# Kernel tuning notes

Measured on AMD Instinct MI355X. Metric: run time of the kernel, lower is better.

## Reference

```python
import jax, jax.numpy as jnp
import numpy as np

HIDDEN = 256
NUM_CLASSES = 96
ENC_FEAT = 256


def setup_inputs() -> dict:
    key = jax.random.key(0)
    ks = jax.random.split(key, 12)
    B, T, D, H, C = 1024, 64, ENC_FEAT, HIDDEN, NUM_CLASSES
    s = 0.05
    return {
        "batch_H": jax.random.normal(ks[0], (B, T, D), jnp.float32),
        "text": jax.random.randint(ks[1], (B, 26), 0, C, jnp.int64),
        "batch_max_length": 25,
        # attention cell params
        "Wi2h": jax.random.normal(ks[2], (D, H), jnp.float32) * s,
        "Wh2h": jax.random.normal(ks[3], (H, H), jnp.float32) * s,
        "bh2h": jnp.zeros((H,), jnp.float32),
        "w_score": jax.random.normal(ks[4], (H, 1), jnp.float32) * s,
        # LSTMCell params (keras gate order: i, f, c, o)
        "Wx": jax.random.normal(ks[5], (D + C, 4 * H), jnp.float32) * s,
        "Wh": jax.random.normal(ks[6], (H, 4 * H), jnp.float32) * s,
        "b_lstm": jnp.concatenate([jnp.zeros((H,)), jnp.ones((H,)), jnp.zeros((2 * H,))]).astype(jnp.float32),
        # generator
        "Wg": jax.random.normal(ks[7], (H, C), jnp.float32) * s,
        "bg": jnp.zeros((C,), jnp.float32),
    }


def _decode(batch_H, text, num_steps, Wi2h, Wh2h, bh2h, w_score, Wx, Wh, b_lstm, Wg, bg):
    B = batch_H.shape[0]
    H = Wh.shape[0]
    C = Wg.shape[1]
    # precompute encoder projection once: [B, T, H]
    batch_H_proj = jnp.einsum("btd,dh->bth", batch_H, Wi2h)

    def step(carry, char_idx):
        h, c = carry
        onehot = jax.nn.one_hot(char_idx, C, dtype=batch_H.dtype)  # [B, C]
        # Bahdanau score: tanh(Wi2h*H + Wh2h*h) @ w_score -> [B, T, 1]
        hp = (h @ Wh2h + bh2h)[:, None, :]
        e = jnp.tanh(batch_H_proj + hp) @ w_score
        alpha = jax.nn.softmax(e, axis=1)  # [B, T, 1]
        context = jnp.sum(alpha * batch_H, axis=1)  # [B, D]
        x = jnp.concatenate([context, onehot], axis=1)  # [B, D+C]
        gates = x @ Wx + h @ Wh + b_lstm  # [B, 4H]
        i_g, f_g, g_g, o_g = jnp.split(gates, 4, axis=1)
        c_new = jax.nn.sigmoid(f_g) * c + jax.nn.sigmoid(i_g) * jnp.tanh(g_g)
        h_new = jax.nn.sigmoid(o_g) * jnp.tanh(c_new)
        return (h_new, c_new), h_new

    h0 = jnp.zeros((B, H), batch_H.dtype)
    c0 = jnp.zeros((B, H), batch_H.dtype)
    chars = text[:, :num_steps].T  # [num_steps, B]
    _, hiddens = jax.lax.scan(step, (h0, c0), chars)
    output_hiddens = jnp.transpose(hiddens, (1, 0, 2))  # [B, num_steps, H]
    probs = output_hiddens @ Wg + bg  # [B, num_steps, C]
    return probs


def reference(batch_H, text, batch_max_length, Wi2h, Wh2h, bh2h, w_score, Wx, Wh, b_lstm, Wg, bg):
    num_steps = batch_max_length + 1
    return _decode(batch_H, text, num_steps, Wi2h, Wh2h, bh2h, w_score, Wx, Wh, b_lstm, Wg, bg)
```

## Files before the change

### kernel.cpp

```cpp
#include <hip/hip_runtime.h>
#include <hip/hip_bf16.h>

constexpr int B  = 1024;
constexpr int T  = 64;
constexpr int D  = 256;
constexpr int H  = 256;
constexpr int C  = 96;
constexpr int NS = 26;
constexpr int G  = 4 * H;

__device__ __forceinline__ float fsig(float x) {
    return __builtin_amdgcn_rcpf(1.0f + __expf(-x));
}
__device__ __forceinline__ float ftanh(float x) {
    float e = __expf(2.0f * x);
    return fmaf(-2.0f, __builtin_amdgcn_rcpf(e + 1.0f), 1.0f);
}
__device__ __forceinline__ float bf_lo(unsigned int p) {
    union { unsigned int i; float f; } v;
    v.i = p << 16;
    return v.f;
}
__device__ __forceinline__ float bf_hi(unsigned int p) {
    union { unsigned int i; float f; } v;
    v.i = p & 0xFFFF0000u;
    return v.f;
}
__device__ __forceinline__ unsigned short f2bf(float f) {
    __hip_bfloat16 h = __float2bfloat16(f);
    return *reinterpret_cast<unsigned short*>(&h);
}

__global__ __launch_bounds__(256) void cvt_kernel(
        const float* __restrict__ in, ushort* __restrict__ out) {
    const int i = blockIdx.x * 256 + threadIdx.x;
    const float4 v = reinterpret_cast<const float4*>(in)[i];
    ushort4 o;
    o.x = f2bf(v.x); o.y = f2bf(v.y); o.z = f2bf(v.z); o.w = f2bf(v.w);
    reinterpret_cast<ushort4*>(out)[i] = o;
}

__global__ __launch_bounds__(256) void proj_kernel(
        const float* __restrict__ bH, const float* __restrict__ Wi2h,
        ushort* __restrict__ proj) {
    __shared__ float xs[32 * 256];
    const int row0 = blockIdx.x * 32;
    const int tid = threadIdx.x;

    const float4* src = reinterpret_cast<const float4*>(bH + (size_t)row0 * D);
    float4* dst = reinterpret_cast<float4*>(xs);
#pragma unroll
    for (int i = 0; i < 8; ++i) dst[tid + 256 * i] = src[tid + 256 * i];
    __syncthreads();

    const int wv = tid >> 6, lane = tid & 63;
    const int r0 = wv * 8;
    const int c0 = lane * 4;
    float4 acc[8];
#pragma unroll
    for (int r = 0; r < 8; ++r) acc[r] = make_float4(0.f, 0.f, 0.f, 0.f);

    for (int k = 0; k < D; k += 4) {
        const float4 w0 = *reinterpret_cast<const float4*>(&Wi2h[(k + 0) * H + c0]);
        const float4 w1 = *reinterpret_cast<const float4*>(&Wi2h[(k + 1) * H + c0]);
        const float4 w2 = *reinterpret_cast<const float4*>(&Wi2h[(k + 2) * H + c0]);
        const float4 w3 = *reinterpret_cast<const float4*>(&Wi2h[(k + 3) * H + c0]);
#pragma unroll
        for (int r = 0; r < 8; ++r) {
            const float4 x = *reinterpret_cast<const float4*>(&xs[(r0 + r) * 256 + k]);
            acc[r].x = fmaf(x.x, w0.x, fmaf(x.y, w1.x, fmaf(x.z, w2.x, fmaf(x.w, w3.x, acc[r].x))));
            acc[r].y = fmaf(x.x, w0.y, fmaf(x.y, w1.y, fmaf(x.z, w2.y, fmaf(x.w, w3.y, acc[r].y))));
            acc[r].z = fmaf(x.x, w0.z, fmaf(x.y, w1.z, fmaf(x.z, w2.z, fmaf(x.w, w3.z, acc[r].z))));
            acc[r].w = fmaf(x.x, w0.w, fmaf(x.y, w1.w, fmaf(x.z, w2.w, fmaf(x.w, w3.w, acc[r].w))));
        }
    }
#pragma unroll
    for (int r = 0; r < 8; ++r) {
        const int brow = row0 + r0 + r;
        const int bb = brow >> 6, tt = brow & 63;
        ushort4 o;
        o.x = f2bf(acc[r].x); o.y = f2bf(acc[r].y);
        o.z = f2bf(acc[r].z); o.w = f2bf(acc[r].w);
        *reinterpret_cast<ushort4*>(
            &proj[(size_t)bb * H * T + (c0 >> 3) * (T * 8) + tt * 8 + (c0 & 7)]) = o;
    }
}

__global__ __launch_bounds__(512, 2) void decoder_kernel(
        const ushort* __restrict__ proj, const ushort* __restrict__ bHb,
        const int* __restrict__ text, const float* __restrict__ Wx,
        const float* __restrict__ Wh, const float* __restrict__ b_lstm,
        const float* __restrict__ Wh2h, const float* __restrict__ bh2h,
        const float* __restrict__ w_score, float* __restrict__ hiddens) {
    __shared__ float hp_s[4][256];
    __shared__ float h_s[4][256];
    __shared__ float c_s[4][256];
    __shared__ float ctx_s[4][256];
    __shared__ float gates[4][1024];
    __shared__ float alpha_s[4][64];
    __shared__ float ws_s[256];

    const int row0 = blockIdx.x * 4;
    const int tid = threadIdx.x;
    const int wv = tid >> 6, lane = tid & 63;

    for (int i = tid; i < 1024; i += 512) {
        const int r = i >> 8, j = i & 255;
        h_s[r][j] = 0.0f;
        c_s[r][j] = 0.0f;
        hp_s[r][j] = bh2h[j];
    }
    if (tid < 256) ws_s[tid] = w_score[tid];
    __syncthreads();

    for (int t = 0; t < NS; ++t) {
        if (wv < 4) {
            const int r = wv;
            const ushort* pb = proj + (size_t)(row0 + r) * H * T + lane * 8;
            float e = 0.0f;
#pragma unroll 4
            for (int h = 0; h < H; h += 8) {
                const uint4 pv = *reinterpret_cast<const uint4*>(pb + (h >> 3) * (T * 8));
                const float4 hp0 = *reinterpret_cast<const float4*>(&hp_s[r][h]);
                const float4 hp1 = *reinterpret_cast<const float4*>(&hp_s[r][h + 4]);
                const float4 w0 = *reinterpret_cast<const float4*>(&ws_s[h]);
                const float4 w1 = *reinterpret_cast<const float4*>(&ws_s[h + 4]);
                e += ftanh(bf_lo(pv.x) + hp0.x) * w0.x;
                e += ftanh(bf_hi(pv.x) + hp0.y) * w0.y;
                e += ftanh(bf_lo(pv.y) + hp0.z) * w0.z;
                e += ftanh(bf_hi(pv.y) + hp0.w) * w0.w;
                e += ftanh(bf_lo(pv.z) + hp1.x) * w1.x;
                e += ftanh(bf_hi(pv.z) + hp1.y) * w1.y;
                e += ftanh(bf_lo(pv.w) + hp1.z) * w1.z;
                e += ftanh(bf_hi(pv.w) + hp1.w) * w1.w;
            }
            {
                float m = e;
#pragma unroll
                for (int off = 32; off > 0; off >>= 1) m = fmaxf(m, __shfl_xor(m, off));
                const float p = __expf(e - m);
                float sum = p;
#pragma unroll
                for (int off = 32; off > 0; off >>= 1) sum += __shfl_xor(sum, off);
                alpha_s[r][lane] = p * __builtin_amdgcn_rcpf(sum);
            }
            {
                const ushort* xb = bHb + (size_t)(row0 + r) * T * D + lane * 4;
                float4 cacc = make_float4(0.f, 0.f, 0.f, 0.f);
#pragma unroll 8
                for (int tt = 0; tt < T; ++tt) {
                    const ushort4 x4 = *reinterpret_cast<const ushort4*>(xb + tt * D);
                    const float av = alpha_s[r][tt];
                    cacc.x = fmaf(av, bf_lo((unsigned)x4.x), cacc.x);
                    cacc.y = fmaf(av, bf_lo((unsigned)x4.y), cacc.y);
                    cacc.z = fmaf(av, bf_lo((unsigned)x4.z), cacc.z);
                    cacc.w = fmaf(av, bf_lo((unsigned)x4.w), cacc.w);
                }
                *reinterpret_cast<float4*>(&ctx_s[r][lane * 4]) = cacc;
            }
        } else {
            const int cw = (wv - 4) * 256 + lane * 4;
            float4 a0, a1, a2, a3;
            {
                const float4 bb = *reinterpret_cast<const float4*>(&b_lstm[cw]);
                const int ch0 = text[(row0 + 0) * NS + t];
                const int ch1 = text[(row0 + 1) * NS + t];
                const int ch2 = text[(row0 + 2) * NS + t];
                const int ch3 = text[(row0 + 3) * NS + t];
                const float4 o0 = *reinterpret_cast<const float4*>(&Wx[(size_t)(D + ch0) * G + cw]);
                const float4 o1 = *reinterpret_cast<const float4*>(&Wx[(size_t)(D + ch1) * G + cw]);
                const float4 o2 = *reinterpret_cast<const float4*>(&Wx[(size_t)(D + ch2) * G + cw]);
                const float4 o3 = *reinterpret_cast<const float4*>(&Wx[(size_t)(D + ch3) * G + cw]);
                a0 = make_float4(bb.x + o0.x, bb.y + o0.y, bb.z + o0.z, bb.w + o0.w);
                a1 = make_float4(bb.x + o1.x, bb.y + o1.y, bb.z + o1.z, bb.w + o1.w);
                a2 = make_float4(bb.x + o2.x, bb.y + o2.y, bb.z + o2.z, bb.w + o2.w);
                a3 = make_float4(bb.x + o3.x, bb.y + o3.y, bb.z + o3.z, bb.w + o3.w);
            }
            for (int k = 0; k < H; k += 4) {
                const float4 w0 = *reinterpret_cast<const float4*>(&Wh[(size_t)(k + 0) * G + cw]);
                const float4 w1 = *reinterpret_cast<const float4*>(&Wh[(size_t)(k + 1) * G + cw]);
                const float4 w2 = *reinterpret_cast<const float4*>(&Wh[(size_t)(k + 2) * G + cw]);
                const float4 w3 = *reinterpret_cast<const float4*>(&Wh[(size_t)(k + 3) * G + cw]);
                const float4 x0 = *reinterpret_cast<const float4*>(&h_s[0][k]);
                const float4 x1 = *reinterpret_cast<const float4*>(&h_s[1][k]);
                const float4 x2 = *reinterpret_cast<const float4*>(&h_s[2][k]);
                const float4 x3 = *reinterpret_cast<const float4*>(&h_s[3][k]);
#define ACC4(A, X)                                                              \
    A.x = fmaf(X.x, w0.x, fmaf(X.y, w1.x, fmaf(X.z, w2.x, fmaf(X.w, w3.x, A.x)))); \
    A.y = fmaf(X.x, w0.y, fmaf(X.y, w1.y, fmaf(X.z, w2.y, fmaf(X.w, w3.y, A.y)))); \
    A.z = fmaf(X.x, w0.z, fmaf(X.y, w1.z, fmaf(X.z, w2.z, fmaf(X.w, w3.z, A.z)))); \
    A.w = fmaf(X.x, w0.w, fmaf(X.y, w1.w, fmaf(X.z, w2.w, fmaf(X.w, w3.w, A.w))))
                ACC4(a0, x0);
                ACC4(a1, x1);
                ACC4(a2, x2);
                ACC4(a3, x3);
#undef ACC4
            }
            *reinterpret_cast<float4*>(&gates[0][cw]) = a0;
            *reinterpret_cast<float4*>(&gates[1][cw]) = a1;
            *reinterpret_cast<float4*>(&gates[2][cw]) = a2;
            *reinterpret_cast<float4*>(&gates[3][cw]) = a3;
        }
        __syncthreads();

        {
            const int cw = wv * 128 + lane * 2;
            float2 a0 = *reinterpret_cast<float2*>(&gates[0][cw]);
            float2 a1 = *reinterpret_cast<float2*>(&gates[1][cw]);
            float2 a2 = *reinterpret_cast<float2*>(&gates[2][cw]);
            float2 a3 = *reinterpret_cast<float2*>(&gates[3][cw]);
            for (int k = 0; k < D; k += 4) {
                const float2 w0 = *reinterpret_cast<const float2*>(&Wx[(size_t)(k + 0) * G + cw]);
                const float2 w1 = *reinterpret_cast<const float2*>(&Wx[(size_t)(k + 1) * G + cw]);
                const float2 w2 = *reinterpret_cast<const float2*>(&Wx[(size_t)(k + 2) * G + cw]);
                const float2 w3 = *reinterpret_cast<const float2*>(&Wx[(size_t)(k + 3) * G + cw]);
                const float4 x0 = *reinterpret_cast<const float4*>(&ctx_s[0][k]);
                const float4 x1 = *reinterpret_cast<const float4*>(&ctx_s[1][k]);
                const float4 x2 = *reinterpret_cast<const float4*>(&ctx_s[2][k]);
                const float4 x3 = *reinterpret_cast<const float4*>(&ctx_s[3][k]);
#define ACC2(A, X)                                                              \
    A.x = fmaf(X.x, w0.x, fmaf(X.y, w1.x, fmaf(X.z, w2.x, fmaf(X.w, w3.x, A.x)))); \
    A.y = fmaf(X.x, w0.y, fmaf(X.y, w1.y, fmaf(X.z, w2.y, fmaf(X.w, w3.y, A.y))))
                ACC2(a0, x0);
                ACC2(a1, x1);
                ACC2(a2, x2);
                ACC2(a3, x3);
#undef ACC2
            }
            *reinterpret_cast<float2*>(&gates[0][cw]) = a0;
            *reinterpret_cast<float2*>(&gates[1][cw]) = a1;
            *reinterpret_cast<float2*>(&gates[2][cw]) = a2;
            *reinterpret_cast<float2*>(&gates[3][cw]) = a3;
        }
        __syncthreads();

#pragma unroll
        for (int pp = 0; pp < 2; ++pp) {
            const int r = (tid >> 8) + pp * 2;
            const int j = tid & 255;
            const float gi = gates[r][j];
            const float gf = gates[r][256 + j];
            const float gc = gates[r][512 + j];
            const float go = gates[r][768 + j];
            const float cv = fsig(gf) * c_s[r][j] + fsig(gi) * ftanh(gc);
            c_s[r][j] = cv;
            const float hvv = fsig(go) * ftanh(cv);
            h_s[r][j] = hvv;
            hiddens[((size_t)(row0 + r) * NS + t) * H + j] = hvv;
        }
        __syncthreads();

        {
            const int j = tid & 255;
            const int rb = (tid >> 8) * 2;
            float acc0 = bh2h[j];
            float acc1 = acc0;
            for (int k = 0; k < H; k += 4) {
                const float w0 = Wh2h[(k + 0) * H + j];
                const float w1 = Wh2h[(k + 1) * H + j];
                const float w2 = Wh2h[(k + 2) * H + j];
                const float w3 = Wh2h[(k + 3) * H + j];
                const float4 xa = *reinterpret_cast<const float4*>(&h_s[rb][k]);
                const float4 xb = *reinterpret_cast<const float4*>(&h_s[rb + 1][k]);
                acc0 = fmaf(xa.x, w0, fmaf(xa.y, w1, fmaf(xa.z, w2, fmaf(xa.w, w3, acc0))));
                acc1 = fmaf(xb.x, w0, fmaf(xb.y, w1, fmaf(xb.z, w2, fmaf(xb.w, w3, acc1))));
            }
            hp_s[rb][j] = acc0;
            hp_s[rb + 1][j] = acc1;
        }
        __syncthreads();
    }
}

__global__ __launch_bounds__(192) void gen_kernel(
        const float* __restrict__ hiddens, const float* __restrict__ Wg,
        const float* __restrict__ bg, float* __restrict__ out) {
    const int row0 = blockIdx.x * 16 + (threadIdx.x / 96) * 8;
    const int cc = threadIdx.x % 96;
    float acc[8];
    const float bias = bg[cc];
#pragma unroll
    for (int r = 0; r < 8; ++r) acc[r] = bias;
    for (int k = 0; k < H; k += 4) {
        const float w0 = Wg[(k + 0) * C + cc];
        const float w1 = Wg[(k + 1) * C + cc];
        const float w2 = Wg[(k + 2) * C + cc];
        const float w3 = Wg[(k + 3) * C + cc];
#pragma unroll
        for (int r = 0; r < 8; ++r) {
            const float4 x = *reinterpret_cast<const float4*>(
                &hiddens[(size_t)(row0 + r) * H + k]);
            acc[r] = fmaf(x.x, w0, acc[r]);
            acc[r] = fmaf(x.y, w1, acc[r]);
            acc[r] = fmaf(x.z, w2, acc[r]);
            acc[r] = fmaf(x.w, w3, acc[r]);
        }
    }
#pragma unroll
    for (int r = 0; r < 8; ++r) out[(size_t)(row0 + r) * C + cc] = acc[r];
}

extern "C" void kernel_launch(void* const* d_in, const int* in_sizes, int n_in,
                              void* d_out, int out_size, void* d_ws, size_t ws_size,
                              hipStream_t stream) {
    const float* batch_H = (const float*)d_in[0];
    const int*   text    = (const int*)d_in[1];
    const float* Wi2h    = (const float*)d_in[3];
    const float* Wh2h    = (const float*)d_in[4];
    const float* bh2h    = (const float*)d_in[5];
    const float* w_score = (const float*)d_in[6];
    const float* Wx      = (const float*)d_in[7];
    const float* Wh      = (const float*)d_in[8];
    const float* b_lstm  = (const float*)d_in[9];
    const float* Wg      = (const float*)d_in[10];
    const float* bg      = (const float*)d_in[11];
    float* out = (float*)d_out;

    char* wsb = (char*)d_ws;
    ushort* proj_bf = (ushort*)wsb;
    ushort* bH_bf   = (ushort*)(wsb + (size_t)B * T * H * 2);
    float*  hiddens = (float*)(wsb + (size_t)B * T * H * 2 * 2);

    cvt_kernel<<<B * T * D / 4 / 256, 256, 0, stream>>>(batch_H, bH_bf);
    proj_kernel<<<B * T / 32, 256, 0, stream>>>(batch_H, Wi2h, proj_bf);
    decoder_kernel<<<B / 4, 512, 0, stream>>>(proj_bf, bH_bf, text, Wx, Wh, b_lstm,
                                              Wh2h, bh2h, w_score, hiddens);
    gen_kernel<<<B * NS / 16, 192, 0, stream>>>(hiddens, Wg, bg, out);
}
```

Baseline: 1.406 ms.

## Pack LSTM weights to bf16 k-pairs and split Wx GEMV across all warps

Adds a pre-pass that converts Wh and the context rows of Wx into bf16, interleaved in k-pairs, so each lane loads 4 columns × 2 k-values in one 16-byte load. Both LSTM gate matvecs in the decoder now read this packed bf16 weight with 8-deep load batching, halving weight bytes streamed per step. The Wx context product is split over k between two warp halves, with a new shared partial buffer summed in the cell update. Unroll factors also increase in the score and Wh2h loops. This risks bf16 rounding error in the recurrent weights and adds shared memory that may affect occupancy.

```diff
diff --git a/kernel.cpp b/kernel.cpp
--- a/kernel.cpp
+++ b/kernel.cpp
@@ -38,6 +38,16 @@
     ushort4 o;
     o.x = f2bf(v.x); o.y = f2bf(v.y); o.z = f2bf(v.z); o.w = f2bf(v.w);
     reinterpret_cast<ushort4*>(out)[i] = o;
+}
+
+__global__ __launch_bounds__(256) void pack_w_kernel(
+        const float* __restrict__ W, ushort* __restrict__ P) {
+    const int i = blockIdx.x * 256 + threadIdx.x;
+    const int k2 = i >> 10, col = i & 1023;
+    ushort2 o;
+    o.x = f2bf(W[(size_t)(2 * k2) * G + col]);
+    o.y = f2bf(W[(size_t)(2 * k2 + 1) * G + col]);
+    *reinterpret_cast<ushort2*>(&P[(size_t)i * 2]) = o;
 }
 
 __global__ __launch_bounds__(256) void proj_kernel(
@@ -89,14 +99,16 @@
 __global__ __launch_bounds__(512, 2) void decoder_kernel(
         const ushort* __restrict__ proj, const ushort* __restrict__ bHb,
         const int* __restrict__ text, const float* __restrict__ Wx,
-        const float* __restrict__ Wh, const float* __restrict__ b_lstm,
-        const float* __restrict__ Wh2h, const float* __restrict__ bh2h,
-        const float* __restrict__ w_score, float* __restrict__ hiddens) {
+        const ushort* __restrict__ WhP, const ushort* __restrict__ WxP,
+        const float* __restrict__ b_lstm, const float* __restrict__ Wh2h,
+        const float* __restrict__ bh2h, const float* __restrict__ w_score,
+        float* __restrict__ hiddens) {
     __shared__ float hp_s[4][256];
     __shared__ float h_s[4][256];
     __shared__ float c_s[4][256];
     __shared__ float ctx_s[4][256];
     __shared__ float gates[4][1024];
+    __shared__ float gpart[4][1024];
     __shared__ float alpha_s[4][64];
     __shared__ float ws_s[256];
 
@@ -118,7 +130,7 @@
             const int r = wv;
             const ushort* pb = proj + (size_t)(row0 + r) * H * T + lane * 8;
             float e = 0.0f;
-#pragma unroll 4
+#pragma unroll 8
             for (int h = 0; h < H; h += 8) {
                 const uint4 pv = *reinterpret_cast<const uint4*>(pb + (h >> 3) * (T * 8));
                 const float4 hp0 = *reinterpret_cast<const float4*>(&hp_s[r][h]);
@@ -176,25 +188,31 @@
                 a2 = make_float4(bb.x + o2.x, bb.y + o2.y, bb.z + o2.z, bb.w + o2.w);
                 a3 = make_float4(bb.x + o3.x, bb.y + o3.y, bb.z + o3.z, bb.w + o3.w);
             }
-            for (int k = 0; k < H; k += 4) {
-                const float4 w0 = *reinterpret_cast<const float4*>(&Wh[(size_t)(k + 0) * G + cw]);
-                const float4 w1 = *reinterpret_cast<const float4*>(&Wh[(size_t)(k + 1) * G + cw]);
-                const float4 w2 = *reinterpret_cast<const float4*>(&Wh[(size_t)(k + 2) * G + cw]);
-                const float4 w3 = *reinterpret_cast<const float4*>(&Wh[(size_t)(k + 3) * G + cw]);
-                const float4 x0 = *reinterpret_cast<const float4*>(&h_s[0][k]);
-                const float4 x1 = *reinterpret_cast<const float4*>(&h_s[1][k]);
-                const float4 x2 = *reinterpret_cast<const float4*>(&h_s[2][k]);
-                const float4 x3 = *reinterpret_cast<const float4*>(&h_s[3][k]);
-#define ACC4(A, X)                                                              \
-    A.x = fmaf(X.x, w0.x, fmaf(X.y, w1.x, fmaf(X.z, w2.x, fmaf(X.w, w3.x, A.x)))); \
-    A.y = fmaf(X.x, w0.y, fmaf(X.y, w1.y, fmaf(X.z, w2.y, fmaf(X.w, w3.y, A.y)))); \
-    A.z = fmaf(X.x, w0.z, fmaf(X.y, w1.z, fmaf(X.z, w2.z, fmaf(X.w, w3.z, A.z)))); \
-    A.w = fmaf(X.x, w0.w, fmaf(X.y, w1.w, fmaf(X.z, w2.w, fmaf(X.w, w3.w, A.w))))
-                ACC4(a0, x0);
-                ACC4(a1, x1);
-                ACC4(a2, x2);
-                ACC4(a3, x3);
-#undef ACC4
+            const ushort* wp = WhP + (size_t)cw * 2;
+            for (int kc = 0; kc < 128; kc += 8) {
+                uint4 pv[8];
+#pragma unroll
+                for (int u = 0; u < 8; ++u)
+                    pv[u] = *reinterpret_cast<const uint4*>(wp + (size_t)(kc + u) * 2048);
+#pragma unroll
+                for (int u = 0; u < 8; ++u) {
+                    const int k0 = (kc + u) * 2;
+                    const float2 x0 = *reinterpret_cast<const float2*>(&h_s[0][k0]);
+                    const float2 x1 = *reinterpret_cast<const float2*>(&h_s[1][k0]);
+                    const float2 x2 = *reinterpret_cast<const float2*>(&h_s[2][k0]);
+                    const float2 x3 = *reinterpret_cast<const float2*>(&h_s[3][k0]);
+                    const float wl0 = bf_lo(pv[u].x), whh0 = bf_hi(pv[u].x);
+                    const float wl1 = bf_lo(pv[u].y), whh1 = bf_hi(pv[u].y);
+                    const float wl2 = bf_lo(pv[u].z), whh2 = bf_hi(pv[u].z);
+                    const float wl3 = bf_lo(pv[u].w), whh3 = bf_hi(pv[u].w);
+#define GACC(A, X)                                      \
+    A.x = fmaf(X.x, wl0, fmaf(X.y, whh0, A.x));         \
+    A.y = fmaf(X.x, wl1, fmaf(X.y, whh1, A.y));         \
+    A.z = fmaf(X.x, wl2, fmaf(X.y, whh2, A.z));         \
+    A.w = fmaf(X.x, wl3, fmaf(X.y, whh3, A.w));
+                    GACC(a0, x0) GACC(a1, x1) GACC(a2, x2) GACC(a3, x3)
+#undef GACC
+                }
             }
             *reinterpret_cast<float4*>(&gates[0][cw]) = a0;
             *reinterpret_cast<float4*>(&gates[1][cw]) = a1;
@@ -204,33 +222,49 @@
         __syncthreads();
 
         {
-            const int cw = wv * 128 + lane * 2;
-            float2 a0 = *reinterpret_cast<float2*>(&gates[0][cw]);
-            float2 a1 = *reinterpret_cast<float2*>(&gates[1][cw]);
-            float2 a2 = *reinterpret_cast<float2*>(&gates[2][cw]);
-            float2 a3 = *reinterpret_cast<float2*>(&gates[3][cw]);
-            for (int k = 0; k < D; k += 4) {
-                const float2 w0 = *reinterpret_cast<const float2*>(&Wx[(size_t)(k + 0) * G + cw]);
-                const float2 w1 = *reinterpret_cast<const float2*>(&Wx[(size_t)(k + 1) * G + cw]);
-                const float2 w2 = *reinterpret_cast<const float2*>(&Wx[(size_t)(k + 2) * G + cw]);
-                const float2 w3 = *reinterpret_cast<const float2*>(&Wx[(size_t)(k + 3) * G + cw]);
-                const float4 x0 = *reinterpret_cast<const float4*>(&ctx_s[0][k]);
-                const float4 x1 = *reinterpret_cast<const float4*>(&ctx_s[1][k]);
-                const float4 x2 = *reinterpret_cast<const float4*>(&ctx_s[2][k]);
-                const float4 x3 = *reinterpret_cast<const float4*>(&ctx_s[3][k]);
-#define ACC2(A, X)                                                              \
-    A.x = fmaf(X.x, w0.x, fmaf(X.y, w1.x, fmaf(X.z, w2.x, fmaf(X.w, w3.x, A.x)))); \
-    A.y = fmaf(X.x, w0.y, fmaf(X.y, w1.y, fmaf(X.z, w2.y, fmaf(X.w, w3.y, A.y))))
-                ACC2(a0, x0);
-                ACC2(a1, x1);
-                ACC2(a2, x2);
-                ACC2(a3, x3);
-#undef ACC2
-            }
-            *reinterpret_cast<float2*>(&gates[0][cw]) = a0;
-            *reinterpret_cast<float2*>(&gates[1][cw]) = a1;
-            *reinterpret_cast<float2*>(&gates[2][cw]) = a2;
-            *reinterpret_cast<float2*>(&gates[3][cw]) = a3;
+            const int cw2 = (wv & 3) * 256 + lane * 4;
+            const int kb = (wv < 4) ? 0 : 64;
+            float4 b0 = make_float4(0.f, 0.f, 0.f, 0.f), b1 = b0, b2 = b0, b3 = b0;
+            const ushort* wp = WxP + (size_t)cw2 * 2 + (size_t)kb * 2048;
+            for (int kc = 0; kc < 64; kc += 8) {
+                uint4 pv[8];
+#pragma unroll
+                for (int u = 0; u < 8; ++u)
+                    pv[u] = *reinterpret_cast<const uint4*>(wp + (size_t)(kc + u) * 2048);
+#pragma unroll
+                for (int u = 0; u < 8; ++u) {
+                    const int k0 = (kb + kc + u) * 2;
+                    const float2 x0 = *reinterpret_cast<const float2*>(&ctx_s[0][k0]);
+                    const float2 x1 = *reinterpret_cast<const float2*>(&ctx_s[1][k0]);
+                    const float2 x2 = *reinterpret_cast<const float2*>(&ctx_s[2][k0]);
+                    const float2 x3 = *reinterpret_cast<const float2*>(&ctx_s[3][k0]);
+                    const float wl0 = bf_lo(pv[u].x), whh0 = bf_hi(pv[u].x);
+                    const float wl1 = bf_lo(pv[u].y), whh1 = bf_hi(pv[u].y);
+                    const float wl2 = bf_lo(pv[u].z), whh2 = bf_hi(pv[u].z);
+                    const float wl3 = bf_lo(pv[u].w), whh3 = bf_hi(pv[u].w);
+#define GACC(A, X)                                      \
+    A.x = fmaf(X.x, wl0, fmaf(X.y, whh0, A.x));         \
+    A.y = fmaf(X.x, wl1, fmaf(X.y, whh1, A.y));         \
+    A.z = fmaf(X.x, wl2, fmaf(X.y, whh2, A.z));         \
+    A.w = fmaf(X.x, wl3, fmaf(X.y, whh3, A.w));
+                    GACC(b0, x0) GACC(b1, x1) GACC(b2, x2) GACC(b3, x3)
+#undef GACC
+                }
+            }
+            if (wv < 4) {
+#pragma unroll
+                for (int r = 0; r < 4; ++r) {
+                    const float4 br = (r == 0) ? b0 : (r == 1) ? b1 : (r == 2) ? b2 : b3;
+                    float4 g = *reinterpret_cast<float4*>(&gates[r][cw2]);
+                    g.x += br.x; g.y += br.y; g.z += br.z; g.w += br.w;
+                    *reinterpret_cast<float4*>(&gates[r][cw2]) = g;
+                }
+            } else {
+                *reinterpret_cast<float4*>(&gpart[0][cw2]) = b0;
+                *reinterpret_cast<float4*>(&gpart[1][cw2]) = b1;
+                *reinterpret_cast<float4*>(&gpart[2][cw2]) = b2;
+                *reinterpret_cast<float4*>(&gpart[3][cw2]) = b3;
+            }
         }
         __syncthreads();
 
@@ -238,10 +272,10 @@
         for (int pp = 0; pp < 2; ++pp) {
             const int r = (tid >> 8) + pp * 2;
             const int j = tid & 255;
-            const float gi = gates[r][j];
-            const float gf = gates[r][256 + j];
-            const float gc = gates[r][512 + j];
-            const float go = gates[r][768 + j];
+            const float gi = gates[r][j] + gpart[r][j];
+            const float gf = gates[r][256 + j] + gpart[r][256 + j];
+            const float gc = gates[r][512 + j] + gpart[r][512 + j];
+            const float go = gates[r][768 + j] + gpart[r][768 + j];
             const float cv = fsig(gf) * c_s[r][j] + fsig(gi) * ftanh(gc);
             c_s[r][j] = cv;
             const float hvv = fsig(go) * ftanh(cv);
@@ -255,6 +289,7 @@
             const int rb = (tid >> 8) * 2;
             float acc0 = bh2h[j];
             float acc1 = acc0;
+#pragma unroll 4
             for (int k = 0; k < H; k += 4) {
                 const float w0 = Wh2h[(k + 0) * H + j];
                 const float w1 = Wh2h[(k + 1) * H + j];
@@ -320,10 +355,15 @@
     ushort* proj_bf = (ushort*)wsb;
     ushort* bH_bf   = (ushort*)(wsb + (size_t)B * T * H * 2);
     float*  hiddens = (float*)(wsb + (size_t)B * T * H * 2 * 2);
+    ushort* WhP     = (ushort*)(wsb + (size_t)B * T * H * 2 * 2 +
+                                (size_t)B * NS * H * 4);
+    ushort* WxP     = WhP + (size_t)(H / 2) * G * 2;
 
     cvt_kernel<<<B * T * D / 4 / 256, 256, 0, stream>>>(batch_H, bH_bf);
+    pack_w_kernel<<<(H / 2) * G / 256, 256, 0, stream>>>(Wh, WhP);
+    pack_w_kernel<<<(D / 2) * G / 256, 256, 0, stream>>>(Wx, WxP);
     proj_kernel<<<B * T / 32, 256, 0, stream>>>(batch_H, Wi2h, proj_bf);
-    decoder_kernel<<<B / 4, 512, 0, stream>>>(proj_bf, bH_bf, text, Wx, Wh, b_lstm,
-                                              Wh2h, bh2h, w_score, hiddens);
+    decoder_kernel<<<B / 4, 512, 0, stream>>>(proj_bf, bH_bf, text, Wx, WhP, WxP,
+                                              b_lstm, Wh2h, bh2h, w_score, hiddens);
     gen_kernel<<<B * NS / 16, 192, 0, stream>>>(hiddens, Wg, bg, out);
 }
```

Measured after the change: 1.278 ms. 9.1% less time.

## Use bf16 MFMA with hi/lo split for decoder recurrent matmuls

Applied to the files above, without the earlier changes.

Replaces the scalar FP32 FMA loops for the Wh, Wx-context and Wh2h matmuls inside the decoder step with 16x16x32 bf16 MFMA instructions. Weights are pre-packed into fragment layout by a new pack kernel, and activations are split into bf16 hi and lo parts stored in swizzled shared memory so that near-FP32 accuracy is kept. The bias and one-hot contributions move into the elementwise gate stage. This is meant to cut per-step ALU and weight-load cost. In exchange it doubles the MFMA work through the hi/lo split and pads the 4-row tiles up to 16 rows, so most of each MFMA is wasted.

```diff
diff --git a/kernel.cpp b/kernel.cpp
--- a/kernel.cpp
+++ b/kernel.cpp
@@ -9,6 +9,11 @@
 constexpr int NS = 26;
 constexpr int G  = 4 * H;
 
+typedef __attribute__((ext_vector_type(8))) short short8v;
+typedef __attribute__((ext_vector_type(4))) float f32x4;
+
+#define MFMA16 __builtin_amdgcn_mfma_f32_16x16x32_bf16
+
 __device__ __forceinline__ float fsig(float x) {
     return __builtin_amdgcn_rcpf(1.0f + __expf(-x));
 }
@@ -17,14 +22,10 @@
     return fmaf(-2.0f, __builtin_amdgcn_rcpf(e + 1.0f), 1.0f);
 }
 __device__ __forceinline__ float bf_lo(unsigned int p) {
-    union { unsigned int i; float f; } v;
-    v.i = p << 16;
-    return v.f;
+    union { unsigned int i; float f; } v; v.i = p << 16; return v.f;
 }
 __device__ __forceinline__ float bf_hi(unsigned int p) {
-    union { unsigned int i; float f; } v;
-    v.i = p & 0xFFFF0000u;
-    return v.f;
+    union { unsigned int i; float f; } v; v.i = p & 0xFFFF0000u; return v.f;
 }
 __device__ __forceinline__ unsigned short f2bf(float f) {
     __hip_bfloat16 h = __float2bfloat16(f);
@@ -38,6 +39,22 @@
     ushort4 o;
     o.x = f2bf(v.x); o.y = f2bf(v.y); o.z = f2bf(v.z); o.w = f2bf(v.w);
     reinterpret_cast<ushort4*>(out)[i] = o;
+}
+
+__global__ __launch_bounds__(256) void pack_frag_kernel(
+        const float* __restrict__ W, ushort* __restrict__ WF,
+        int ncol_tiles, int wstride) {
+    const int i = blockIdx.x * 256 + threadIdx.x;
+    const int l = i & 63;
+    const int s = (i >> 6) & 7;
+    const int ct = i >> 9;
+    if (ct >= ncol_tiles) return;
+    const int col = ct * 16 + (l & 15);
+    const int k0 = s * 32 + (l >> 4) * 8;
+    ushort o[8];
+#pragma unroll
+    for (int j = 0; j < 8; ++j) o[j] = f2bf(W[(size_t)(k0 + j) * wstride + col]);
+    *reinterpret_cast<uint4*>(&WF[(size_t)i * 8]) = *reinterpret_cast<uint4*>(o);
 }
 
 __global__ __launch_bounds__(256) void proj_kernel(
@@ -86,27 +103,54 @@
     }
 }
 
+__device__ __forceinline__ short8v ldA(const ushort* base, int lane, int s) {
+    const int row = lane & 15, g = lane >> 4;
+    const int byte = ((row << 9) + (s << 6) + (g << 4)) ^ ((row & 7) << 4);
+    return *reinterpret_cast<const short8v*>(
+        reinterpret_cast<const char*>(base) + byte);
+}
+__device__ __forceinline__ void loadB(short8v dst[8], const ushort* __restrict__ wf,
+                                      int ctg, int lane) {
+#pragma unroll
+    for (int s = 0; s < 8; ++s)
+        dst[s] = *reinterpret_cast<const short8v*>(
+            wf + (((size_t)ctg * 8 + s) * 64 + lane) * 8);
+}
+__device__ __forceinline__ f32x4 mfma_hilo(const short8v aHi[8], const short8v aLo[8],
+                                           const short8v b[8]) {
+    f32x4 acc = {0.f, 0.f, 0.f, 0.f};
+#pragma unroll
+    for (int s = 0; s < 8; ++s) {
+        acc = MFMA16(aLo[s], b[s], acc, 0, 0, 0);
+        acc = MFMA16(aHi[s], b[s], acc, 0, 0, 0);
+    }
+    return acc;
+}
+
 __global__ __launch_bounds__(512, 2) void decoder_kernel(
         const ushort* __restrict__ proj, const ushort* __restrict__ bHb,
         const int* __restrict__ text, const float* __restrict__ Wx,
-        const float* __restrict__ Wh, const float* __restrict__ b_lstm,
-        const float* __restrict__ Wh2h, const float* __restrict__ bh2h,
-        const float* __restrict__ w_score, float* __restrict__ hiddens) {
+        const ushort* __restrict__ WhF, const ushort* __restrict__ WxF,
+        const ushort* __restrict__ Wh2hF, const float* __restrict__ b_lstm,
+        const float* __restrict__ bh2h, const float* __restrict__ w_score,
+        float* __restrict__ hiddens) {
     __shared__ float hp_s[4][256];
-    __shared__ float h_s[4][256];
     __shared__ float c_s[4][256];
-    __shared__ float ctx_s[4][256];
     __shared__ float gates[4][1024];
     __shared__ float alpha_s[4][64];
     __shared__ float ws_s[256];
+    __shared__ ushort hHi[16 * 256], hLo[16 * 256];
+    __shared__ ushort cHi[16 * 256], cLo[16 * 256];
 
     const int row0 = blockIdx.x * 4;
     const int tid = threadIdx.x;
     const int wv = tid >> 6, lane = tid & 63;
 
+    for (int i = tid; i < 4096; i += 512) {
+        hHi[i] = 0; hLo[i] = 0; cHi[i] = 0; cLo[i] = 0;
+    }
     for (int i = tid; i < 1024; i += 512) {
         const int r = i >> 8, j = i & 255;
-        h_s[r][j] = 0.0f;
         c_s[r][j] = 0.0f;
         hp_s[r][j] = bh2h[j];
     }
@@ -118,7 +162,7 @@
             const int r = wv;
             const ushort* pb = proj + (size_t)(row0 + r) * H * T + lane * 8;
             float e = 0.0f;
-#pragma unroll 4
+#pragma unroll 8
             for (int h = 0; h < H; h += 8) {
                 const uint4 pv = *reinterpret_cast<const uint4*>(pb + (h >> 3) * (T * 8));
                 const float4 hp0 = *reinterpret_cast<const float4*>(&hp_s[r][h]);
@@ -156,81 +200,66 @@
                     cacc.z = fmaf(av, bf_lo((unsigned)x4.z), cacc.z);
                     cacc.w = fmaf(av, bf_lo((unsigned)x4.w), cacc.w);
                 }
-                *reinterpret_cast<float4*>(&ctx_s[r][lane * 4]) = cacc;
+                ushort4 hi, lo;
+                hi.x = f2bf(cacc.x); lo.x = f2bf(cacc.x - bf_lo((unsigned)hi.x));
+                hi.y = f2bf(cacc.y); lo.y = f2bf(cacc.y - bf_lo((unsigned)hi.y));
+                hi.z = f2bf(cacc.z); lo.z = f2bf(cacc.z - bf_lo((unsigned)hi.z));
+                hi.w = f2bf(cacc.w); lo.w = f2bf(cacc.w - bf_lo((unsigned)hi.w));
+                const int byte = ((r << 9) + (lane << 3)) ^ ((r & 7) << 4);
+                *reinterpret_cast<ushort4*>(reinterpret_cast<char*>(cHi) + byte) = hi;
+                *reinterpret_cast<ushort4*>(reinterpret_cast<char*>(cLo) + byte) = lo;
             }
         } else {
-            const int cw = (wv - 4) * 256 + lane * 4;
-            float4 a0, a1, a2, a3;
-            {
-                const float4 bb = *reinterpret_cast<const float4*>(&b_lstm[cw]);
-                const int ch0 = text[(row0 + 0) * NS + t];
-                const int ch1 = text[(row0 + 1) * NS + t];
-                const int ch2 = text[(row0 + 2) * NS + t];
-                const int ch3 = text[(row0 + 3) * NS + t];
-                const float4 o0 = *reinterpret_cast<const float4*>(&Wx[(size_t)(D + ch0) * G + cw]);
-                const float4 o1 = *reinterpret_cast<const float4*>(&Wx[(size_t)(D + ch1) * G + cw]);
-                const float4 o2 = *reinterpret_cast<const float4*>(&Wx[(size_t)(D + ch2) * G + cw]);
-                const float4 o3 = *reinterpret_cast<const float4*>(&Wx[(size_t)(D + ch3) * G + cw]);
-                a0 = make_float4(bb.x + o0.x, bb.y + o0.y, bb.z + o0.z, bb.w + o0.w);
-                a1 = make_float4(bb.x + o1.x, bb.y + o1.y, bb.z + o1.z, bb.w + o1.w);
-                a2 = make_float4(bb.x + o2.x, bb.y + o2.y, bb.z + o2.z, bb.w + o2.w);
-                a3 = make_float4(bb.x + o3.x, bb.y + o3.y, bb.z + o3.z, bb.w + o3.w);
-            }
-            for (int k = 0; k < H; k += 4) {
-                const float4 w0 = *reinterpret_cast<const float4*>(&Wh[(size_t)(k + 0) * G + cw]);
-                const float4 w1 = *reinterpret_cast<const float4*>(&Wh[(size_t)(k + 1) * G + cw]);
-                const float4 w2 = *reinterpret_cast<const float4*>(&Wh[(size_t)(k + 2) * G + cw]);
-                const float4 w3 = *reinterpret_cast<const float4*>(&Wh[(size_t)(k + 3) * G + cw]);
-                const float4 x0 = *reinterpret_cast<const float4*>(&h_s[0][k]);
-                const float4 x1 = *reinterpret_cast<const float4*>(&h_s[1][k]);
-                const float4 x2 = *reinterpret_cast<const float4*>(&h_s[2][k]);
-                const float4 x3 = *reinterpret_cast<const float4*>(&h_s[3][k]);
-#define ACC4(A, X)                                                              \
-    A.x = fmaf(X.x, w0.x, fmaf(X.y, w1.x, fmaf(X.z, w2.x, fmaf(X.w, w3.x, A.x)))); \
-    A.y = fmaf(X.x, w0.y, fmaf(X.y, w1.y, fmaf(X.z, w2.y, fmaf(X.w, w3.y, A.y)))); \
-    A.z = fmaf(X.x, w0.z, fmaf(X.y, w1.z, fmaf(X.z, w2.z, fmaf(X.w, w3.z, A.z)))); \
-    A.w = fmaf(X.x, w0.w, fmaf(X.y, w1.w, fmaf(X.z, w2.w, fmaf(X.w, w3.w, A.w))))
-                ACC4(a0, x0);
-                ACC4(a1, x1);
-                ACC4(a2, x2);
-                ACC4(a3, x3);
-#undef ACC4
-            }
-            *reinterpret_cast<float4*>(&gates[0][cw]) = a0;
-            *reinterpret_cast<float4*>(&gates[1][cw]) = a1;
-            *reinterpret_cast<float4*>(&gates[2][cw]) = a2;
-            *reinterpret_cast<float4*>(&gates[3][cw]) = a3;
+            short8v aHi[8], aLo[8];
+#pragma unroll
+            for (int s = 0; s < 8; ++s) { aHi[s] = ldA(hHi, lane, s); aLo[s] = ldA(hLo, lane, s); }
+            const int ct0 = (wv - 4) * 16;
+            short8v bA[8], bB[8];
+            loadB(bA, WhF, ct0, lane);
+#pragma unroll
+            for (int ct = 0; ct < 16; ct += 2) {
+                loadB(bB, WhF, ct0 + ct + 1, lane);
+                f32x4 acc = mfma_hilo(aHi, aLo, bA);
+                if (lane < 16) {
+                    const int col = (ct0 + ct) * 16 + lane;
+                    gates[0][col] = acc[0]; gates[1][col] = acc[1];
+                    gates[2][col] = acc[2]; gates[3][col] = acc[3];
+                }
+                if (ct + 2 < 16) loadB(bA, WhF, ct0 + ct + 2, lane);
+                acc = mfma_hilo(aHi, aLo, bB);
+                if (lane < 16) {
+                    const int col = (ct0 + ct + 1) * 16 + lane;
+                    gates[0][col] = acc[0]; gates[1][col] = acc[1];
+                    gates[2][col] = acc[2]; gates[3][col] = acc[3];
+                }
+            }
         }
         __syncthreads();
 
         {
-            const int cw = wv * 128 + lane * 2;
-            float2 a0 = *reinterpret_cast<float2*>(&gates[0][cw]);
-            float2 a1 = *reinterpret_cast<float2*>(&gates[1][cw]);
-            float2 a2 = *reinterpret_cast<float2*>(&gates[2][cw]);
-            float2 a3 = *reinterpret_cast<float2*>(&gates[3][cw]);
-            for (int k = 0; k < D; k += 4) {
-                const float2 w0 = *reinterpret_cast<const float2*>(&Wx[(size_t)(k + 0) * G + cw]);
-                const float2 w1 = *reinterpret_cast<const float2*>(&Wx[(size_t)(k + 1) * G + cw]);
-                const float2 w2 = *reinterpret_cast<const float2*>(&Wx[(size_t)(k + 2) * G + cw]);
-                const float2 w3 = *reinterpret_cast<const float2*>(&Wx[(size_t)(k + 3) * G + cw]);
-                const float4 x0 = *reinterpret_cast<const float4*>(&ctx_s[0][k]);
-                const float4 x1 = *reinterpret_cast<const float4*>(&ctx_s[1][k]);
-                const float4 x2 = *reinterpret_cast<const float4*>(&ctx_s[2][k]);
-                const float4 x3 = *reinterpret_cast<const float4*>(&ctx_s[3][k]);
-#define ACC2(A, X)                                                              \
-    A.x = fmaf(X.x, w0.x, fmaf(X.y, w1.x, fmaf(X.z, w2.x, fmaf(X.w, w3.x, A.x)))); \
-    A.y = fmaf(X.x, w0.y, fmaf(X.y, w1.y, fmaf(X.z, w2.y, fmaf(X.w, w3.y, A.y))))
-                ACC2(a0, x0);
-                ACC2(a1, x1);
-                ACC2(a2, x2);
-                ACC2(a3, x3);
-#undef ACC2
-            }
-            *reinterpret_cast<float2*>(&gates[0][cw]) = a0;
-            *reinterpret_cast<float2*>(&gates[1][cw]) = a1;
-            *reinterpret_cast<float2*>(&gates[2][cw]) = a2;
-            *reinterpret_cast<float2*>(&gates[3][cw]) = a3;
+            short8v aHi[8], aLo[8];
+#pragma unroll
+            for (int s = 0; s < 8; ++s) { aHi[s] = ldA(cHi, lane, s); aLo[s] = ldA(cLo, lane, s); }
+            const int ct0 = wv * 8;
+            short8v bA[8], bB[8];
+            loadB(bA, WxF, ct0, lane);
+#pragma unroll
+            for (int ct = 0; ct < 8; ct += 2) {
+                loadB(bB, WxF, ct0 + ct + 1, lane);
+                f32x4 acc = mfma_hilo(aHi, aLo, bA);
+                if (lane < 16) {
+                    const int col = (ct0 + ct) * 16 + lane;
+                    gates[0][col] += acc[0]; gates[1][col] += acc[1];
+                    gates[2][col] += acc[2]; gates[3][col] += acc[3];
+                }
+                if (ct + 2 < 8) loadB(bA, WxF, ct0 + ct + 2, lane);
+                acc = mfma_hilo(aHi, aLo, bB);
+                if (lane < 16) {
+                    const int col = (ct0 + ct + 1) * 16 + lane;
+                    gates[0][col] += acc[0]; gates[1][col] += acc[1];
+                    gates[2][col] += acc[2]; gates[3][col] += acc[3];
+                }
+            }
         }
         __syncthreads();
 
@@ -238,35 +267,43 @@
         for (int pp = 0; pp < 2; ++pp) {
             const int r = (tid >> 8) + pp * 2;
             const int j = tid & 255;
-            const float gi = gates[r][j];
-            const float gf = gates[r][256 + j];
-            const float gc = gates[r][512 + j];
-            const float go = gates[r][768 + j];
+            const int ch = text[(row0 + r) * NS + t];
+            const float* oh = Wx + (size_t)(D + ch) * G;
+            const float gi = gates[r][j]       + b_lstm[j]       + oh[j];
+            const float gf = gates[r][256 + j] + b_lstm[256 + j] + oh[256 + j];
+            const float gc = gates[r][512 + j] + b_lstm[512 + j] + oh[512 + j];
+            const float go = gates[r][768 + j] + b_lstm[768 + j] + oh[768 + j];
             const float cv = fsig(gf) * c_s[r][j] + fsig(gi) * ftanh(gc);
             c_s[r][j] = cv;
             const float hvv = fsig(go) * ftanh(cv);
-            h_s[r][j] = hvv;
             hiddens[((size_t)(row0 + r) * NS + t) * H + j] = hvv;
+            const ushort hi = f2bf(hvv);
+            const ushort lo = f2bf(hvv - bf_lo((unsigned)hi));
+            const int byte = ((r << 9) + (j << 1)) ^ ((r & 7) << 4);
+            *reinterpret_cast<ushort*>(reinterpret_cast<char*>(hHi) + byte) = hi;
+            *reinterpret_cast<ushort*>(reinterpret_cast<char*>(hLo) + byte) = lo;
         }
         __syncthreads();
 
         {
-            const int j = tid & 255;
-            const int rb = (tid >> 8) * 2;
-            float acc0 = bh2h[j];
-            float acc1 = acc0;
-            for (int k = 0; k < H; k += 4) {
-                const float w0 = Wh2h[(k + 0) * H + j];
-                const float w1 = Wh2h[(k + 1) * H + j];
-                const float w2 = Wh2h[(k + 2) * H + j];
-                const float w3 = Wh2h[(k + 3) * H + j];
-                const float4 xa = *reinterpret_cast<const float4*>(&h_s[rb][k]);
-                const float4 xb = *reinterpret_cast<const float4*>(&h_s[rb + 1][k]);
-                acc0 = fmaf(xa.x, w0, fmaf(xa.y, w1, fmaf(xa.z, w2, fmaf(xa.w, w3, acc0))));
-                acc1 = fmaf(xb.x, w0, fmaf(xb.y, w1, fmaf(xb.z, w2, fmaf(xb.w, w3, acc1))));
-            }
-            hp_s[rb][j] = acc0;
-            hp_s[rb + 1][j] = acc1;
+            short8v aHi[8], aLo[8];
+#pragma unroll
+            for (int s = 0; s < 8; ++s) { aHi[s] = ldA(hHi, lane, s); aLo[s] = ldA(hLo, lane, s); }
+            short8v b0[8], b1[8];
+            loadB(b0, Wh2hF, wv * 2 + 0, lane);
+            loadB(b1, Wh2hF, wv * 2 + 1, lane);
+            f32x4 acc0 = mfma_hilo(aHi, aLo, b0);
+            f32x4 acc1 = mfma_hilo(aHi, aLo, b1);
+            if (lane < 16) {
+                int col = (wv * 2 + 0) * 16 + lane;
+                float bb = bh2h[col];
+                hp_s[0][col] = acc0[0] + bb; hp_s[1][col] = acc0[1] + bb;
+                hp_s[2][col] = acc0[2] + bb; hp_s[3][col] = acc0[3] + bb;
+                col = (wv * 2 + 1) * 16 + lane;
+                bb = bh2h[col];
+                hp_s[0][col] = acc1[0] + bb; hp_s[1][col] = acc1[1] + bb;
+                hp_s[2][col] = acc1[2] + bb; hp_s[3][col] = acc1[3] + bb;
+            }
         }
         __syncthreads();
     }
@@ -320,10 +357,17 @@
     ushort* proj_bf = (ushort*)wsb;
     ushort* bH_bf   = (ushort*)(wsb + (size_t)B * T * H * 2);
     float*  hiddens = (float*)(wsb + (size_t)B * T * H * 2 * 2);
+    ushort* WhF     = (ushort*)(wsb + (size_t)B * T * H * 2 * 2 +
+                                (size_t)B * NS * H * 4);
+    ushort* WxF     = WhF + (size_t)256 * 1024;
+    ushort* Wh2hF   = WxF + (size_t)256 * 1024;
 
     cvt_kernel<<<B * T * D / 4 / 256, 256, 0, stream>>>(batch_H, bH_bf);
+    pack_frag_kernel<<<128, 256, 0, stream>>>(Wh, WhF, 64, G);
+    pack_frag_kernel<<<128, 256, 0, stream>>>(Wx, WxF, 64, G);
+    pack_frag_kernel<<<32, 256, 0, stream>>>(Wh2h, Wh2hF, 16, H);
     proj_kernel<<<B * T / 32, 256, 0, stream>>>(batch_H, Wi2h, proj_bf);
-    decoder_kernel<<<B / 4, 512, 0, stream>>>(proj_bf, bH_bf, text, Wx, Wh, b_lstm,
-                                              Wh2h, bh2h, w_score, hiddens);
+    decoder_kernel<<<B / 4, 512, 0, stream>>>(proj_bf, bH_bf, text, Wx, WhF, WxF,
+                                              Wh2hF, b_lstm, bh2h, w_score, hiddens);
     gen_kernel<<<B * NS / 16, 192, 0, stream>>>(hiddens, Wg, bg, out);
 }
```

New measurement: 2.363 ms. 68.1% more time.
